# Kernel tuning notes

Hardware: AMD Instinct MI355X
Metric: run time of the kernel (lower is better)

Reference implementation:

```python
import jax, jax.numpy as jnp
import numpy as np

B, S, T, D_IN, D_T = 32, 4096, 8192, 128, 256


def _length_mask(key, batch, maxlen, minlen):
    lens = jax.random.randint(key, (batch,), minlen, maxlen + 1)
    lens = lens.at[0].set(maxlen)  # ensure max(t_lens)==maxlen (static t_len)
    return (jnp.arange(maxlen)[None, :] < lens[:, None]).astype(jnp.float32)


def setup_inputs() -> dict:
    key = jax.random.key(0)
    ks = jax.random.split(key, 8)
    student_emb = jax.random.normal(ks[0], (B, S, D_IN), dtype=jnp.float32)
    s_mask = _length_mask(ks[1], B, S, S // 2)
    t_mask = _length_mask(ks[2], B, T, T // 2)
    # params (stored as [in, out] so y = x @ W + b)
    pe_w1 = jax.random.normal(ks[3], (1, 64), dtype=jnp.float32) * 0.1
    pe_b1 = jnp.zeros((64,), dtype=jnp.float32)
    pe_w2 = jax.random.normal(ks[4], (64, D_IN), dtype=jnp.float32) * 0.1
    pe_b2 = jnp.zeros((D_IN,), dtype=jnp.float32)
    pt_w = jax.random.normal(ks[5], (2 * D_IN, D_T), dtype=jnp.float32) * 0.05
    pt_b = jnp.zeros((D_T,), dtype=jnp.float32)
    ln_g = jnp.ones((D_T,), dtype=jnp.float32)
    ln_b = jnp.zeros((D_T,), dtype=jnp.float32)
    neighbor_weights = jnp.ones((3,), dtype=jnp.float32)
    return {
        "student_emb": student_emb, "s_mask": s_mask, "t_mask": t_mask,
        "target_length": T,
        "pe_w1": pe_w1, "pe_b1": pe_b1, "pe_w2": pe_w2, "pe_b2": pe_b2,
        "pt_w": pt_w, "pt_b": pt_b, "ln_g": ln_g, "ln_b": ln_b,
        "neighbor_weights": neighbor_weights,
    }


def _layernorm(x, g, b, eps=1e-5):
    mu = jnp.mean(x, axis=-1, keepdims=True)
    var = jnp.mean(jnp.square(x - mu), axis=-1, keepdims=True)
    return (x - mu) * jax.lax.rsqrt(var + eps) * g + b


def reference(student_emb, s_mask, t_mask, target_length,
              pe_w1, pe_b1, pe_w2, pe_b2, pt_w, pt_b, ln_g, ln_b,
              neighbor_weights):
    batch, s_len, _ = student_emb.shape
    t_len = t_mask.shape[1]  # == max(t_mask.sum(1)) by construction
    s_lens = s_mask.sum(axis=1)  # [B] float
    pos = jnp.linspace(0.0, 1.0, t_len)  # [T]
    pos_grid = jnp.broadcast_to(pos[None, :], (batch, t_len))
    s_pos = pos_grid * (s_lens[:, None] - 1.0)
    curr = s_pos.astype(jnp.int32)                      # floor (nonneg)
    prev = jnp.clip(curr - 1, 0, s_len - 1)
    nxt = jnp.clip(curr + 1, 0, s_len - 1)

    def gat(idx):  # masked gather: [B,T,D]
        e = jnp.take_along_axis(student_emb, idx[..., None], axis=1)
        m = jnp.take_along_axis(s_mask, idx, axis=1)[..., None]
        return e * m

    w = jax.nn.softmax(neighbor_weights)
    blended = w[0] * gat(prev) + w[1] * gat(curr) + w[2] * gat(nxt)

    # position encoder MLP on scalar positions
    h = jax.nn.gelu(pos_grid[..., None] * pe_w1[0] + pe_b1, approximate=False)
    pos_emb = h @ pe_w2 + pe_b2  # [B,T,D_in]

    combined = jnp.concatenate([blended, pos_emb], axis=-1)  # [B,T,2*D_in]
    trans = jax.nn.gelu(combined @ pt_w + pt_b, approximate=False)
    trans = _layernorm(trans, ln_g, ln_b)
    trans = trans * t_mask[:, :t_len, None]
    if t_len < target_length:
        trans = jnp.pad(trans, ((0, 0), (0, target_length - t_len), (0, 0)))
    return trans
```

## Files before the change

### kernel.cpp

```cpp
#include <hip/hip_runtime.h>
#include <math.h>

#define S_LEN 4096
#define T_LEN 8192
#define D_TT  256
#define TILE_M 32
#define NKT   6
#define LDA   264

typedef unsigned short u16;
typedef __attribute__((ext_vector_type(8))) unsigned short u16x8;
typedef __attribute__((ext_vector_type(4))) float f32x4;
typedef __bf16 bf16x8 __attribute__((ext_vector_type(8)));

__device__ __forceinline__ float bf2f(u16 v) {
    union { unsigned u; float f; } x; x.u = ((unsigned)v) << 16; return x.f;
}
__device__ __forceinline__ u16 f2bf(float f) {
    __bf16 h = (__bf16)f;
    union { __bf16 h; u16 u; } x; x.h = h; return x.u;
}
__device__ __forceinline__ float gelu_f(float x) {
    return 0.5f * x * (1.0f + erff(x * 0.70710678118654752440f));
}
__device__ __forceinline__ float gelu_fast(float x) {
    float z = fabsf(x) * 0.70710678118654752440f;
    float t = __builtin_amdgcn_rcpf(fmaf(0.3275911f, z, 1.0f));
    float p = fmaf(t, 1.061405429f, -1.453152027f);
    p = fmaf(t, p, 1.421413741f);
    p = fmaf(t, p, -0.284496736f);
    p = fmaf(t, p, 0.254829592f);
    p = p * t;
    float e = __expf(-z * z);
    float er = fmaf(-p, e, 1.0f);
    er = copysignf(er, x);
    return 0.5f * x * (1.0f + er);
}

__device__ __forceinline__ bool detect_f32(const void* t_mask) {
    return *(const unsigned*)t_mask == 0x3F800000u;
}

template<bool F32>
__device__ __forceinline__ float ld1(const void* p, size_t i) {
    if constexpr (F32) return ((const float*)p)[i];
    else return bf2f(((const u16*)p)[i]);
}
template<bool F32>
__device__ __forceinline__ void load8(const void* p, size_t idx, float o[8]) {
    if constexpr (F32) {
        const float4* q = (const float4*)((const float*)p + idx);
        float4 a = q[0], b = q[1];
        o[0]=a.x; o[1]=a.y; o[2]=a.z; o[3]=a.w;
        o[4]=b.x; o[5]=b.y; o[6]=b.z; o[7]=b.w;
    } else {
        u16x8 v = *(const u16x8*)((const u16*)p + idx);
        #pragma unroll
        for (int j = 0; j < 8; ++j) o[j] = bf2f(v[j]);
    }
}
template<bool F32>
__device__ __forceinline__ void store8(void* p, size_t idx, const float o[8]) {
    if constexpr (F32) {
        float4 a = {o[0],o[1],o[2],o[3]};
        float4 b = {o[4],o[5],o[6],o[7]};
        float4* q = (float4*)((float*)p + idx);
        q[0] = a; q[1] = b;
    } else {
        u16x8 v;
        #pragma unroll
        for (int j = 0; j < 8; ++j) v[j] = f2bf(o[j]);
        *(u16x8*)((u16*)p + idx) = v;
    }
}


template<bool F32>
__global__ __launch_bounds__(256) void prep_kernel(
    const void* __restrict__ s_mask, const void* __restrict__ t_mask_det,
    const void* __restrict__ nw,
    const void* __restrict__ pe_w2, const void* __restrict__ pe_b2,
    const void* __restrict__ pt_w, const void* __restrict__ pt_b,
    int* __restrict__ ws_len, float* __restrict__ ws_w,
    float* __restrict__ ws_bias, u16* __restrict__ ws_bfrag)
{
    if (detect_f32(t_mask_det) != F32) return;
    int bi = blockIdx.x;
    int tid = threadIdx.x;
    if (bi < 32) {
        __shared__ float red[256];
        float s = 0.f;
        for (int i = tid; i < S_LEN; i += 256) s += ld1<F32>(s_mask, (size_t)bi * S_LEN + i);
        red[tid] = s;
        __syncthreads();
        for (int off = 128; off > 0; off >>= 1) {
            if (tid < off) red[tid] += red[tid + off];
            __syncthreads();
        }
        if (tid == 0) ws_len[bi] = (int)(red[0] + 0.5f);
    } else if (bi == 32) {
        if (tid == 0) {
            float a = ld1<F32>(nw, 0), b = ld1<F32>(nw, 1), c = ld1<F32>(nw, 2);
            float m = fmaxf(a, fmaxf(b, c));
            float ea = expf(a - m), eb = expf(b - m), ec = expf(c - m);
            float inv = 1.0f / (ea + eb + ec);
            ws_w[0] = ea * inv; ws_w[1] = eb * inv; ws_w[2] = ec * inv;
        }
    } else if (bi == 33) {
        int n = tid;
        float acc = ld1<F32>(pt_b, n);
        for (int d = 0; d < 128; ++d)
            acc += ld1<F32>(pe_b2, d) * ld1<F32>(pt_w, (size_t)(128 + d) * D_TT + n);
        ws_bias[n] = acc;
    } else if (bi < 42) {
        __shared__ float pw[8 * 128];
        int j0 = (bi - 34) * 8;
        for (int i = tid; i < 1024; i += 256)
            pw[i] = ld1<F32>(pe_w2, (size_t)j0 * 128 + i);
        __syncthreads();
        int n = tid;
        float acc[8];
        #pragma unroll
        for (int i = 0; i < 8; ++i) acc[i] = 0.f;
        for (int d = 0; d < 128; ++d) {
            float w = ld1<F32>(pt_w, (size_t)(128 + d) * D_TT + n);
            #pragma unroll
            for (int i = 0; i < 8; ++i) acc[i] += pw[i * 128 + d] * w;
        }
        int nt = n >> 4, lm = n & 15;
        #pragma unroll
        for (int i = 0; i < 8; ++i) {
            int j = j0 + i;
            int kt = 4 + (j >> 5);
            int qq = (j >> 3) & 3;
            int jj = j & 7;
            int f = kt * 16 + nt;
            int lane = qq * 16 + lm;
            ws_bfrag[((size_t)f * 64 + lane) * 8 + jj] = f2bf(acc[i]);
        }
    } else {
        int g = (bi - 42) * 256 + tid;
        int f = g >> 6;
        int lane = g & 63;
        int kt = f >> 4, nt = f & 15;
        int q = lane >> 4, lm = lane & 15;
        u16x8 v;
        #pragma unroll
        for (int jj = 0; jj < 8; ++jj) {
            int k = kt * 32 + q * 8 + jj;
            int n = nt * 16 + lm;
            v[jj] = f2bf(ld1<F32>(pt_w, (size_t)k * D_TT + n));
        }
        *(u16x8*)(ws_bfrag + ((size_t)f * 64 + lane) * 8) = v;
    }
}

template<bool F32>
__global__ __launch_bounds__(256, 8) void main_kernel(
    const void* __restrict__ emb, const void* __restrict__ s_mask,
    const void* __restrict__ t_mask,
    const void* __restrict__ pe_w1, const void* __restrict__ pe_b1,
    const void* __restrict__ ln_g, const void* __restrict__ ln_b,
    const int* __restrict__ ws_len, const float* __restrict__ ws_w,
    const float* __restrict__ ws_bias, const u16* __restrict__ ws_bfrag,
    void* __restrict__ out)
{
    if (detect_f32(t_mask) != F32) return;

    __shared__ __align__(16) u16 ldsC[TILE_M * LDA];
    __shared__ float ldsPartS[TILE_M][4];
    __shared__ float ldsPartQ[TILE_M][4];
    __shared__ float ldsMu[TILE_M];
    __shared__ float ldsRstd[TILE_M];

    int tid = threadIdx.x;
    int b = blockIdx.x >> 8;
    int tile = blockIdx.x & 255;
    int t0 = tile * TILE_M;

    int Li = ws_len[b];
    float w0 = ws_w[0], w1 = ws_w[1], w2 = ws_w[2];

    {
        int tt = tid >> 3, sub = tid & 7;
        int t = t0 + tt;
        const float step = 1.0f / 8191.0f;
        float posf = (float)t * step;
        float sp = posf * (float)(Li - 1);
        int ci = (int)sp;
        if (ci > S_LEN - 1) ci = S_LEN - 1;
        int pi = ci - 1; if (pi < 0) pi = 0;
        int ni = ci + 1; if (ni > S_LEN - 1) ni = S_LEN - 1;
        float mp = ld1<F32>(s_mask, (size_t)b * S_LEN + pi);
        float mc = ld1<F32>(s_mask, (size_t)b * S_LEN + ci);
        float mn = ld1<F32>(s_mask, (size_t)b * S_LEN + ni);
        float wp = w0 * mp, wc = w1 * mc, wn = w2 * mn;
        size_t Ep = ((size_t)b * S_LEN + pi) * 128;
        size_t Ec = ((size_t)b * S_LEN + ci) * 128;
        size_t En = ((size_t)b * S_LEN + ni) * 128;
        #pragma unroll
        for (int c = 0; c < 2; ++c) {
            int col = c * 64 + sub * 8;
            float vp[8], vc[8], vn[8];
            load8<F32>(emb, Ep + col, vp);
            load8<F32>(emb, Ec + col, vc);
            load8<F32>(emb, En + col, vn);
            u16x8 o;
            #pragma unroll
            for (int j = 0; j < 8; ++j)
                o[j] = f2bf(wp * vp[j] + wc * vc[j] + wn * vn[j]);
            *(u16x8*)(&ldsC[tt * LDA + col]) = o;
        }
        {
            u16x8 hv;
            #pragma unroll
            for (int jj = 0; jj < 8; ++jj) {
                int j = sub * 8 + jj;
                float x = posf * ld1<F32>(pe_w1, j) + ld1<F32>(pe_b1, j);
                hv[jj] = f2bf(gelu_f(x));
            }
            *(u16x8*)(&ldsC[tt * LDA + 128 + sub * 8]) = hv;
        }
    }
    __syncthreads();

    int lane = tid & 63, wv = tid >> 6;
    int q = lane >> 4, lm = lane & 15;
    f32x4 acc[2][4];
    #pragma unroll
    for (int m = 0; m < 2; ++m)
        #pragma unroll
        for (int n = 0; n < 4; ++n) acc[m][n] = (f32x4){0.f, 0.f, 0.f, 0.f};

    #pragma unroll
    for (int kt = 0; kt < NKT; ++kt) {
        bf16x8 a[2];
        #pragma unroll
        for (int m = 0; m < 2; ++m)
            a[m] = *(const bf16x8*)(&ldsC[(m * 16 + lm) * LDA + kt * 32 + q * 8]);
        #pragma unroll
        for (int n = 0; n < 4; ++n) {
            int nt = wv * 4 + n;
            bf16x8 bf = *(const bf16x8*)(ws_bfrag + ((size_t)(kt * 16 + nt) * 64 + lane) * 8);
            #pragma unroll
            for (int m = 0; m < 2; ++m)
                acc[m][n] = __builtin_amdgcn_mfma_f32_16x16x32_bf16(a[m], bf, acc[m][n], 0, 0, 0);
        }
    }
    __syncthreads();

    float bias[4];
    #pragma unroll
    for (int n = 0; n < 4; ++n) bias[n] = ws_bias[wv * 64 + n * 16 + lm];
    #pragma unroll
    for (int m = 0; m < 2; ++m) {
        int r0 = m * 16 + q * 4;
        float ps[4], pq[4];
        #pragma unroll
        for (int r = 0; r < 4; ++r) { ps[r] = 0.f; pq[r] = 0.f; }
        #pragma unroll
        for (int n = 0; n < 4; ++n)
            #pragma unroll
            for (int r = 0; r < 4; ++r) {
                float g = gelu_fast(acc[m][n][r] + bias[n]);
                ldsC[(r0 + r) * LDA + wv * 64 + n * 16 + lm] = f2bf(g);
                ps[r] += g;
                pq[r] += g * g;
            }
        #pragma unroll
        for (int off = 1; off < 16; off <<= 1)
            #pragma unroll
            for (int r = 0; r < 4; ++r) {
                ps[r] += __shfl_xor(ps[r], off, 16);
                pq[r] += __shfl_xor(pq[r], off, 16);
            }
        if (lm == 0) {
            #pragma unroll
            for (int r = 0; r < 4; ++r) {
                ldsPartS[r0 + r][wv] = ps[r];
                ldsPartQ[r0 + r][wv] = pq[r];
            }
        }
    }
    __syncthreads();
    if (tid < TILE_M) {
        float s  = ldsPartS[tid][0] + ldsPartS[tid][1] + ldsPartS[tid][2] + ldsPartS[tid][3];
        float sq = ldsPartQ[tid][0] + ldsPartQ[tid][1] + ldsPartQ[tid][2] + ldsPartQ[tid][3];
        float mu = s * (1.0f / 256.0f);
        float var = sq * (1.0f / 256.0f) - mu * mu;
        ldsMu[tid] = mu;
        ldsRstd[tid] = rsqrtf(var + 1e-5f);
    }
    __syncthreads();

    {
        int tt = tid >> 3, part = tid & 7;
        float mu = ldsMu[tt], rs = ldsRstd[tt];
        float tm = ld1<F32>(t_mask, (size_t)b * T_LEN + t0 + tt);
        size_t rowbase = (((size_t)b * T_LEN) + t0 + tt) * D_TT;
        #pragma unroll
        for (int c = 0; c < 4; ++c) {
            int col = c * 64 + part * 8;
            u16x8 v = *(u16x8*)(&ldsC[tt * LDA + col]);
            float gv[8], bv[8], o[8];
            load8<F32>(ln_g, col, gv);
            load8<F32>(ln_b, col, bv);
            #pragma unroll
            for (int j = 0; j < 8; ++j) {
                float y = (bf2f(v[j]) - mu) * rs * gv[j] + bv[j];
                o[j] = y * tm;
            }
            store8<F32>(out, rowbase + col, o);
        }
    }
}

extern "C" void kernel_launch(void* const* d_in, const int* in_sizes, int n_in,
                              void* d_out, int out_size, void* d_ws, size_t ws_size,
                              hipStream_t stream)
{
    (void)in_sizes; (void)n_in; (void)out_size; (void)ws_size;
    const void* emb    = d_in[0];
    const void* s_mask = d_in[1];
    const void* t_mask = d_in[2];
    const void* pe_w1  = d_in[4];
    const void* pe_b1  = d_in[5];
    const void* pe_w2  = d_in[6];
    const void* pe_b2  = d_in[7];
    const void* pt_w   = d_in[8];
    const void* pt_b   = d_in[9];
    const void* ln_g   = d_in[10];
    const void* ln_b   = d_in[11];
    const void* nw     = d_in[12];

    char* ws = (char*)d_ws;
    int*   ws_len  = (int*)ws;
    float* ws_w    = (float*)(ws + 128);
    float* ws_bias = (float*)(ws + 256);
    u16*   ws_bfrag= (u16*)(ws + 1280);

    prep_kernel<false><<<58, 256, 0, stream>>>(s_mask, t_mask, nw, pe_w2, pe_b2,
                                               pt_w, pt_b, ws_len, ws_w, ws_bias, ws_bfrag);
    prep_kernel<true><<<58, 256, 0, stream>>>(s_mask, t_mask, nw, pe_w2, pe_b2,
                                              pt_w, pt_b, ws_len, ws_w, ws_bias, ws_bfrag);
    main_kernel<false><<<32 * (T_LEN / TILE_M), 256, 0, stream>>>(
        emb, s_mask, t_mask, pe_w1, pe_b1, ln_g, ln_b,
        ws_len, ws_w, ws_bias, ws_bfrag, d_out);
    main_kernel<true><<<32 * (T_LEN / TILE_M), 256, 0, stream>>>(
        emb, s_mask, t_mask, pe_w1, pe_b1, ln_g, ln_b,
        ws_len, ws_w, ws_bias, ws_bfrag, d_out);
}
```

Measured before the change: 435.4 us.

## Precompute batch-independent positional projection once per position, shrink main GEMM K

The positional-encoder half of the projection depends only on position, not on batch, so it is computed once per target position in a new prep kernel (T×256 fp32 table with bias folded in). The main kernel drops the per-tile GELU positional features and the two positional K-tiles, cutting MFMA work and GELU/erf evaluation by a third of K. In exchange, each output element now reads an extra fp32 value from a 8 MB table (L2/MALL-resident, shared across 32 batches), and an extra kernel launch is added.

```diff
diff --git a/kernel.cpp b/kernel.cpp
--- a/kernel.cpp
+++ b/kernel.cpp
@@ -5,7 +5,7 @@
 #define T_LEN 8192
 #define D_TT  256
 #define TILE_M 32
-#define NKT   6
+#define NKT4  4
 #define LDA   264
 
 typedef unsigned short u16;
@@ -76,13 +76,14 @@
 
 
 template<bool F32>
-__global__ __launch_bounds__(256) void prep_kernel(
+__global__ __launch_bounds__(256) void prep_a(
     const void* __restrict__ s_mask, const void* __restrict__ t_mask_det,
     const void* __restrict__ nw,
     const void* __restrict__ pe_w2, const void* __restrict__ pe_b2,
     const void* __restrict__ pt_w, const void* __restrict__ pt_b,
     int* __restrict__ ws_len, float* __restrict__ ws_w,
-    float* __restrict__ ws_bias, u16* __restrict__ ws_bfrag)
+    float* __restrict__ ws_bias, float* __restrict__ ws_w2p,
+    u16* __restrict__ ws_bfrag)
 {
     if (detect_f32(t_mask_det) != F32) return;
     int bi = blockIdx.x;
@@ -106,38 +107,31 @@
             float inv = 1.0f / (ea + eb + ec);
             ws_w[0] = ea * inv; ws_w[1] = eb * inv; ws_w[2] = ec * inv;
         }
-    } else if (bi == 33) {
+    } else if (bi < 41) {
+        __shared__ float pw[8 * 128];
+        int j0 = (bi - 33) * 8;
+        for (int i = tid; i < 1024; i += 256) pw[i] = ld1<F32>(pe_w2, (size_t)j0 * 128 + i);
+        __syncthreads();
+        int n = tid;
+        float acc[8];
+        #pragma unroll
+        for (int i = 0; i < 8; ++i) acc[i] = 0.f;
+        for (int d = 0; d < 128; ++d) {
+            float w = ld1<F32>(pt_w, (size_t)(128 + d) * D_TT + n);
+            #pragma unroll
+            for (int i = 0; i < 8; ++i) acc[i] += pw[i * 128 + d] * w;
+        }
+        #pragma unroll
+        for (int i = 0; i < 8; ++i) ws_w2p[(size_t)(j0 + i) * D_TT + n] = acc[i];
+    } else if (bi == 41) {
+        __shared__ float pb[128];
+        for (int i = tid; i < 128; i += 256) pb[i] = ld1<F32>(pe_b2, i);
+        __syncthreads();
         int n = tid;
         float acc = ld1<F32>(pt_b, n);
         for (int d = 0; d < 128; ++d)
-            acc += ld1<F32>(pe_b2, d) * ld1<F32>(pt_w, (size_t)(128 + d) * D_TT + n);
+            acc += pb[d] * ld1<F32>(pt_w, (size_t)(128 + d) * D_TT + n);
         ws_bias[n] = acc;
-    } else if (bi < 42) {
-        __shared__ float pw[8 * 128];
-        int j0 = (bi - 34) * 8;
-        for (int i = tid; i < 1024; i += 256)
-            pw[i] = ld1<F32>(pe_w2, (size_t)j0 * 128 + i);
-        __syncthreads();
-        int n = tid;
-        float acc[8];
-        #pragma unroll
-        for (int i = 0; i < 8; ++i) acc[i] = 0.f;
-        for (int d = 0; d < 128; ++d) {
-            float w = ld1<F32>(pt_w, (size_t)(128 + d) * D_TT + n);
-            #pragma unroll
-            for (int i = 0; i < 8; ++i) acc[i] += pw[i * 128 + d] * w;
-        }
-        int nt = n >> 4, lm = n & 15;
-        #pragma unroll
-        for (int i = 0; i < 8; ++i) {
-            int j = j0 + i;
-            int kt = 4 + (j >> 5);
-            int qq = (j >> 3) & 3;
-            int jj = j & 7;
-            int f = kt * 16 + nt;
-            int lane = qq * 16 + lm;
-            ws_bfrag[((size_t)f * 64 + lane) * 8 + jj] = f2bf(acc[i]);
-        }
     } else {
         int g = (bi - 42) * 256 + tid;
         int f = g >> 6;
@@ -156,13 +150,48 @@
 }
 
 template<bool F32>
+__global__ __launch_bounds__(256) void prep_b(
+    const void* __restrict__ t_mask_det,
+    const void* __restrict__ pe_w1, const void* __restrict__ pe_b1,
+    const float* __restrict__ ws_bias, const float* __restrict__ ws_w2p,
+    float* __restrict__ posc)
+{
+    if (detect_f32(t_mask_det) != F32) return;
+    __shared__ float w2[64 * 256];
+    __shared__ float hl[16 * 64];
+    int tid = threadIdx.x;
+    int T0 = blockIdx.x * 16;
+    for (int i = tid; i < 4096; i += 256)
+        ((float4*)w2)[i] = ((const float4*)ws_w2p)[i];
+    for (int k = tid; k < 1024; k += 256) {
+        int tl = k >> 6, j = k & 63;
+        float posf = (float)(T0 + tl) * (1.0f / 8191.0f);
+        float x = posf * ld1<F32>(pe_w1, j) + ld1<F32>(pe_b1, j);
+        hl[k] = gelu_f(x);
+    }
+    __syncthreads();
+    int n = tid;
+    float bias = ws_bias[n];
+    float acc[16];
+    #pragma unroll
+    for (int tl = 0; tl < 16; ++tl) acc[tl] = bias;
+    for (int j = 0; j < 64; ++j) {
+        float w = w2[j * 256 + n];
+        #pragma unroll
+        for (int tl = 0; tl < 16; ++tl) acc[tl] += hl[tl * 64 + j] * w;
+    }
+    #pragma unroll
+    for (int tl = 0; tl < 16; ++tl)
+        posc[(size_t)(T0 + tl) * D_TT + n] = acc[tl];
+}
+
+template<bool F32>
 __global__ __launch_bounds__(256, 8) void main_kernel(
     const void* __restrict__ emb, const void* __restrict__ s_mask,
     const void* __restrict__ t_mask,
-    const void* __restrict__ pe_w1, const void* __restrict__ pe_b1,
     const void* __restrict__ ln_g, const void* __restrict__ ln_b,
     const int* __restrict__ ws_len, const float* __restrict__ ws_w,
-    const float* __restrict__ ws_bias, const u16* __restrict__ ws_bfrag,
+    const u16* __restrict__ ws_bfrag, const float* __restrict__ posc,
     void* __restrict__ out)
 {
     if (detect_f32(t_mask) != F32) return;
@@ -211,16 +240,6 @@
                 o[j] = f2bf(wp * vp[j] + wc * vc[j] + wn * vn[j]);
             *(u16x8*)(&ldsC[tt * LDA + col]) = o;
         }
-        {
-            u16x8 hv;
-            #pragma unroll
-            for (int jj = 0; jj < 8; ++jj) {
-                int j = sub * 8 + jj;
-                float x = posf * ld1<F32>(pe_w1, j) + ld1<F32>(pe_b1, j);
-                hv[jj] = f2bf(gelu_f(x));
-            }
-            *(u16x8*)(&ldsC[tt * LDA + 128 + sub * 8]) = hv;
-        }
     }
     __syncthreads();
 
@@ -233,7 +252,7 @@
         for (int n = 0; n < 4; ++n) acc[m][n] = (f32x4){0.f, 0.f, 0.f, 0.f};
 
     #pragma unroll
-    for (int kt = 0; kt < NKT; ++kt) {
+    for (int kt = 0; kt < NKT4; ++kt) {
         bf16x8 a[2];
         #pragma unroll
         for (int m = 0; m < 2; ++m)
@@ -249,12 +268,10 @@
     }
     __syncthreads();
 
-    float bias[4];
-    #pragma unroll
-    for (int n = 0; n < 4; ++n) bias[n] = ws_bias[wv * 64 + n * 16 + lm];
     #pragma unroll
     for (int m = 0; m < 2; ++m) {
         int r0 = m * 16 + q * 4;
+        const float* pc = posc + ((size_t)(t0 + r0)) * D_TT + wv * 64 + lm;
         float ps[4], pq[4];
         #pragma unroll
         for (int r = 0; r < 4; ++r) { ps[r] = 0.f; pq[r] = 0.f; }
@@ -262,7 +279,7 @@
         for (int n = 0; n < 4; ++n)
             #pragma unroll
             for (int r = 0; r < 4; ++r) {
-                float g = gelu_fast(acc[m][n][r] + bias[n]);
+                float g = gelu_fast(acc[m][n][r] + pc[(size_t)r * D_TT + n * 16]);
                 ldsC[(r0 + r) * LDA + wv * 64 + n * 16 + lm] = f2bf(g);
                 ps[r] += g;
                 pq[r] += g * g;
@@ -334,19 +351,21 @@
     const void* nw     = d_in[12];
 
     char* ws = (char*)d_ws;
-    int*   ws_len  = (int*)ws;
-    float* ws_w    = (float*)(ws + 128);
-    float* ws_bias = (float*)(ws + 256);
-    u16*   ws_bfrag= (u16*)(ws + 1280);
-
-    prep_kernel<false><<<58, 256, 0, stream>>>(s_mask, t_mask, nw, pe_w2, pe_b2,
-                                               pt_w, pt_b, ws_len, ws_w, ws_bias, ws_bfrag);
-    prep_kernel<true><<<58, 256, 0, stream>>>(s_mask, t_mask, nw, pe_w2, pe_b2,
-                                              pt_w, pt_b, ws_len, ws_w, ws_bias, ws_bfrag);
+    int*   ws_len   = (int*)ws;
+    float* ws_w     = (float*)(ws + 128);
+    float* ws_bias  = (float*)(ws + 256);
+    u16*   ws_bfrag = (u16*)(ws + 1280);
+    float* ws_w2p   = (float*)(ws + 66816);
+    float* posc     = (float*)(ws + 132352);
+
+    prep_a<false><<<58, 256, 0, stream>>>(s_mask, t_mask, nw, pe_w2, pe_b2,
+                                          pt_w, pt_b, ws_len, ws_w, ws_bias, ws_w2p, ws_bfrag);
+    prep_a<true><<<58, 256, 0, stream>>>(s_mask, t_mask, nw, pe_w2, pe_b2,
+                                         pt_w, pt_b, ws_len, ws_w, ws_bias, ws_w2p, ws_bfrag);
+    prep_b<false><<<T_LEN / 16, 256, 0, stream>>>(t_mask, pe_w1, pe_b1, ws_bias, ws_w2p, posc);
+    prep_b<true><<<T_LEN / 16, 256, 0, stream>>>(t_mask, pe_w1, pe_b1, ws_bias, ws_w2p, posc);
     main_kernel<false><<<32 * (T_LEN / TILE_M), 256, 0, stream>>>(
-        emb, s_mask, t_mask, pe_w1, pe_b1, ln_g, ln_b,
-        ws_len, ws_w, ws_bias, ws_bfrag, d_out);
+        emb, s_mask, t_mask, ln_g, ln_b, ws_len, ws_w, ws_bfrag, posc, d_out);
     main_kernel<true><<<32 * (T_LEN / TILE_M), 256, 0, stream>>>(
-        emb, s_mask, t_mask, pe_w1, pe_b1, ln_g, ln_b,
-        ws_len, ws_w, ws_bias, ws_bfrag, d_out);
-}
+        emb, s_mask, t_mask, ln_g, ln_b, ws_len, ws_w, ws_bfrag, posc, d_out);
+}
```

Measured after the change: 462.6 us. 1.06x slower.
